# Kernel tuning notes

Hardware: AMD Instinct MI355X
Metric: run time of the kernel (lower is better)

## Reference

```python
import jax, jax.numpy as jnp
import numpy as np
from jax.ops import segment_sum

N_NODES = 100000
N_EDGES = 1600000
IN_DIM, HID_DIM, OUT_DIM = 64, 48, 32


def setup_inputs() -> dict:
    key = jax.random.key(0)
    ks = jax.random.split(key, 4)
    x = jax.random.normal(ks[0], (N_NODES, IN_DIM), dtype=jnp.float32)
    edge_index = jax.random.randint(ks[1], (2, N_EDGES), 0, N_NODES, dtype=jnp.int64)
    W1 = jax.random.normal(ks[2], (IN_DIM, HID_DIM), dtype=jnp.float32) / np.sqrt(IN_DIM)
    b1 = jnp.zeros((HID_DIM,), dtype=jnp.float32)
    W2 = jax.random.normal(ks[3], (HID_DIM, OUT_DIM), dtype=jnp.float32) / np.sqrt(HID_DIM)
    b2 = jnp.zeros((OUT_DIM,), dtype=jnp.float32)
    return {"x": x, "edge_index": edge_index, "W1": W1, "b1": b1, "W2": W2, "b2": b2}


def _gcn_conv(x, W, b, src, dst, deg_inv_sqrt, n_nodes):
    # GCNConv: out = D^{-1/2} (A + I) D^{-1/2} (x W) + b
    h = x @ W                                   # [N, F_out]
    norm = deg_inv_sqrt[src] * deg_inv_sqrt[dst]  # [E+N]
    msg = h[src] * norm[:, None]                # gather + scale
    out = segment_sum(msg, dst, num_segments=n_nodes)  # scatter-add over dst
    return out + b


def reference(x, edge_index, W1, b1, W2, b2):
    n = x.shape[0]
    loop = jnp.arange(n, dtype=edge_index.dtype)
    src = jnp.concatenate([edge_index[0], loop])  # add self-loops (PyG default)
    dst = jnp.concatenate([edge_index[1], loop])
    deg = segment_sum(jnp.ones_like(dst, dtype=x.dtype), dst, num_segments=n)
    deg_inv_sqrt = jnp.where(deg > 0, jax.lax.rsqrt(jnp.maximum(deg, 1.0)), 0.0)
    h = _gcn_conv(x, W1, b1, src, dst, deg_inv_sqrt, n)
    h = jax.nn.relu(h)
    embeddings = _gcn_conv(h, W2, b2, src, dst, deg_inv_sqrt, n)
    return embeddings
```

## Files before the change

kernel.cpp:

```cpp
#include <hip/hip_runtime.h>
#include <hip/hip_fp16.h>


#define NN 100000
#define NE 1600000
#define NPB 128
#define NBUCK ((NN + NPB - 1) / NPB)
#define PBITS 17
#define PMASK ((1 << PBITS) - 1)
#define CHB 3
#define CHS 14
#define NKEY (NPB << CHB)
#define CAP 4096
#define UN 8
#define PART_B 512
#define EPT 8
#define RUNW (PART_B * EPT)
#define PART_G ((NE + RUNW - 1) / RUNW)
#define GROWS 256
#define GEMM_G ((NN + GROWS - 1) / GROWS)
#define GB NBUCK

struct alignas(8)  half4 { __half2 lo, hi; };
struct alignas(16) half8 { __half2 a, b, c, d; };

__global__ __launch_bounds__(512) void
k_lsortgemm(const int* __restrict__ src, const int* __restrict__ dst,
            int* __restrict__ runs, unsigned int* __restrict__ seg,
            const float* __restrict__ X, const float* __restrict__ W1,
            __half* __restrict__ Hh) {
    __shared__ int h[NBUCK];
    __shared__ int tsum[512];
    __shared__ int stage[RUNW];
    __shared__ float w[64 * 48];
    int tid = threadIdx.x;

    if (blockIdx.x < PART_G) {
        for (int i = tid; i < NBUCK; i += PART_B) h[i] = 0;
        __syncthreads();
        int ebase = blockIdx.x * RUNW;
        int pw[EPT], pb[EPT];
#pragma unroll
        for (int k = 0; k < EPT; ++k) {
            int e = ebase + k * PART_B + tid;
            if (e < NE) {
                int d = dst[e];
                pb[k] = d >> 7;
                pw[k] = src[e] | ((d & (NPB - 1)) << PBITS);
                atomicAdd(&h[pb[k]], 1);
            } else pb[k] = -1;
        }
        __syncthreads();
        int c0 = 0, c1 = 0;
        if (tid < NBUCK / 2) { c0 = h[2 * tid]; c1 = h[2 * tid + 1]; }
        int loc = c0 + c1;
        tsum[tid] = (tid < NBUCK / 2) ? loc : 0;
        __syncthreads();
        for (int off = 1; off < 512; off <<= 1) {
            int v = (tid >= off) ? tsum[tid - off] : 0;
            __syncthreads();
            tsum[tid] += v;
            __syncthreads();
        }
        if (tid < NBUCK / 2) {
            int base = tsum[tid] - loc;
            seg[(size_t)blockIdx.x * NBUCK + 2 * tid]     = ((unsigned)base << 9) | (unsigned)c0;
            seg[(size_t)blockIdx.x * NBUCK + 2 * tid + 1] = ((unsigned)(base + c0) << 9) | (unsigned)c1;
            h[2 * tid]     = base;
            h[2 * tid + 1] = base + c0;
        }
        __syncthreads();
#pragma unroll
        for (int k = 0; k < EPT; ++k) {
            if (pb[k] >= 0) {
                int r = atomicAdd(&h[pb[k]], 1);
                stage[r] = pw[k];
            }
        }
        __syncthreads();
#pragma unroll
        for (int k = 0; k < EPT; ++k)
            runs[(size_t)blockIdx.x * RUNW + k * PART_B + tid] = stage[k * PART_B + tid];
        return;
    }

    constexpr int NC = 48, CPT = 12, CG = 4, KF4 = 16;
    int R0 = (blockIdx.x - PART_G) * GROWS;
    for (int i = tid; i < 64 * 48; i += 512) w[i] = W1[i];
    __syncthreads();

    int tc = tid % CG, tr = tid / CG;
    int r0 = R0 + 2 * tr, r1 = r0 + 1;
    int c0 = tc * CPT;
    bool ok0 = r0 < NN, ok1 = r1 < NN;
    const float4* X4 = (const float4*)X;
    const float4 z4 = make_float4(0.f, 0.f, 0.f, 0.f);

    float acc[2][CPT];
#pragma unroll
    for (int rr = 0; rr < 2; ++rr)
#pragma unroll
        for (int j = 0; j < CPT; ++j) acc[rr][j] = 0.f;

#pragma unroll 2
    for (int k4 = 0; k4 < KF4; ++k4) {
        float4 xa = ok0 ? X4[(size_t)r0 * KF4 + k4] : z4;
        float4 xb = ok1 ? X4[(size_t)r1 * KF4 + k4] : z4;
        float ar[4] = {xa.x, xa.y, xa.z, xa.w};
        float br[4] = {xb.x, xb.y, xb.z, xb.w};
#pragma unroll
        for (int j = 0; j < 4; ++j) {
            float va = ar[j], vb = br[j];
#pragma unroll
            for (int q = 0; q < CPT / 4; ++q) {
                float4 wv = *(const float4*)&w[(4 * k4 + j) * NC + c0 + 4 * q];
                acc[0][q*4+0] = fmaf(va, wv.x, acc[0][q*4+0]);
                acc[0][q*4+1] = fmaf(va, wv.y, acc[0][q*4+1]);
                acc[0][q*4+2] = fmaf(va, wv.z, acc[0][q*4+2]);
                acc[0][q*4+3] = fmaf(va, wv.w, acc[0][q*4+3]);
                acc[1][q*4+0] = fmaf(vb, wv.x, acc[1][q*4+0]);
                acc[1][q*4+1] = fmaf(vb, wv.y, acc[1][q*4+1]);
                acc[1][q*4+2] = fmaf(vb, wv.z, acc[1][q*4+2]);
                acc[1][q*4+3] = fmaf(vb, wv.w, acc[1][q*4+3]);
            }
        }
    }
#pragma unroll
    for (int rr = 0; rr < 2; ++rr) {
        int gr = r0 + rr;
        if (gr >= NN) continue;
#pragma unroll
        for (int q = 0; q < CPT / 4; ++q) {
            __half2 p0 = __floats2half2_rn(acc[rr][q*4+0], acc[rr][q*4+1]);
            __half2 p1 = __floats2half2_rn(acc[rr][q*4+2], acc[rr][q*4+3]);
            half4 hv; hv.lo = p0; hv.hi = p1;
            *(half4*)(Hh + (size_t)gr * NC + c0 + 4 * q) = hv;
        }
    }
}

__global__ __launch_bounds__(256) void
k_segt(const unsigned int* __restrict__ seg, unsigned int* __restrict__ segT) {
    __shared__ unsigned int t[32][33];
    constexpr int TX = (NBUCK + 31) / 32;
    int bx = blockIdx.x % TX;
    int by = blockIdx.x / TX;
    int lx = threadIdx.x & 31, ly = threadIdx.x >> 5;
    int bu0 = bx * 32, bl0 = by * 32;
#pragma unroll
    for (int k = 0; k < 32; k += 8) {
        int blk = bl0 + ly + k, bu = bu0 + lx;
        t[ly + k][lx] = (blk < PART_G && bu < NBUCK) ? seg[(size_t)blk * NBUCK + bu] : 0u;
    }
    __syncthreads();
#pragma unroll
    for (int k = 0; k < 32; k += 8) {
        int bu = bu0 + ly + k, blk = bl0 + lx;
        if (bu < NBUCK && blk < PART_G)
            segT[(size_t)bu * PART_G + blk] = t[lx][ly + k];
    }
}

__global__ __launch_bounds__(256) void
k_bsort2(const int* __restrict__ runs, const unsigned int* __restrict__ segT,
         int* __restrict__ srcsort, unsigned int* __restrict__ rowinfo,
         float* __restrict__ dinv, __half* __restrict__ Hh) {
    __shared__ int stage[CAP];
    __shared__ int cnt[NKEY];
    __shared__ int tsum[256];
    __shared__ float sd[NPB];
    int tid = threadIdx.x, b = blockIdx.x;

    unsigned int s0 = (tid < PART_G) ? segT[(size_t)b * PART_G + tid] : 0u;
    unsigned int s1 = (tid + 256 < PART_G) ? segT[(size_t)b * PART_G + tid + 256] : 0u;
    int l0 = (int)(s0 & 511u), l1 = (int)(s1 & 511u);
    int mylen = l0 + l1;
    tsum[tid] = mylen;
    __syncthreads();
    for (int off = 1; off < 256; off <<= 1) {
        int v = (tid >= off) ? tsum[tid - off] : 0;
        __syncthreads();
        tsum[tid] += v;
        __syncthreads();
    }
    int wbase = tsum[tid] - mylen;
    int sz = tsum[255];
    {
        const int* p = runs + (size_t)tid * RUNW + (s0 >> 9);
        for (int i = 0; i < l0; ++i) stage[wbase + i] = p[i];
        p = runs + (size_t)(tid + 256) * RUNW + (s1 >> 9);
        for (int i = 0; i < l1; ++i) stage[wbase + l0 + i] = p[i];
    }
    for (int i = tid; i < NKEY; i += 256) cnt[i] = 0;
    __syncthreads();

    for (int i = tid; i < sz; i += 256) {
        int w = stage[i];
        int key = ((w >> PBITS) << CHB) | ((w & PMASK) >> CHS);
        atomicAdd(&cnt[key], 1);
    }
    __syncthreads();
    int k0 = tid * 4;
    int c0 = cnt[k0], c1 = cnt[k0 + 1], c2 = cnt[k0 + 2], c3 = cnt[k0 + 3];
    int loc = c0 + c1 + c2 + c3;
    tsum[tid] = loc;
    __syncthreads();
    for (int off = 1; off < 256; off <<= 1) {
        int v = (tid >= off) ? tsum[tid - off] : 0;
        __syncthreads();
        tsum[tid] += v;
        __syncthreads();
    }
    int base = tsum[tid] - loc;
    cnt[k0]     = base;
    cnt[k0 + 1] = base + c0;
    cnt[k0 + 2] = base + c0 + c1;
    cnt[k0 + 3] = base + c0 + c1 + c2;
    __syncthreads();
    int e0 = b * CAP;
    if (tid < NPB) {
        int node = b * NPB + tid;
        int rs = cnt[tid << CHB];
        int re = (tid == NPB - 1) ? sz : cnt[(tid + 1) << CHB];
        float dv = rsqrtf((float)(re - rs + 1));
        sd[tid] = dv;
        if (node < NN) {
            rowinfo[node] = ((unsigned int)(e0 + rs) << 10) | (unsigned int)(re - rs);
            dinv[node] = dv;
        }
    }
    __syncthreads();
    for (int i = tid; i < sz; i += 256) {
        int w = stage[i];
        int key = ((w >> PBITS) << CHB) | ((w & PMASK) >> CHS);
        int p = atomicAdd(&cnt[key], 1);
        srcsort[e0 + p] = w & PMASK;
    }
    for (int t = tid; t < NPB * 6; t += 256) {
        int lr = t / 6, q = t - lr * 6;
        int node = b * NPB + lr;
        if (node >= NN) continue;
        float s = sd[lr];
        half8* hp = (half8*)(Hh + (size_t)node * 48 + 8 * q);
        half8 v = *hp;
        float2 f0 = __half22float2(v.a), f1 = __half22float2(v.b);
        float2 f2 = __half22float2(v.c), f3 = __half22float2(v.d);
        v.a = __floats2half2_rn(f0.x * s, f0.y * s);
        v.b = __floats2half2_rn(f1.x * s, f1.y * s);
        v.c = __floats2half2_rn(f2.x * s, f2.y * s);
        v.d = __floats2half2_rn(f3.x * s, f3.y * s);
        *hp = v;
    }
}

__global__ __launch_bounds__(256) void
k_fused48(const __half* __restrict__ Hh, const unsigned int* __restrict__ rowinfo,
          const int* __restrict__ srcsort, const float* __restrict__ dinv,
          const float* __restrict__ b1, const float* __restrict__ W2,
          __half* __restrict__ Hh2) {
    constexpr int ROWS = 128, XS = 49;
    __shared__ float Xs[ROWS * XS];
    __shared__ float w2[48 * 32];
    __shared__ float bb[48];
    int tid = threadIdx.x;
    int R0 = blockIdx.x * ROWS;
    for (int i = tid; i < 48 * 32; i += 256) w2[i] = W2[i];
    if (tid < 48) bb[tid] = b1[tid];
    __syncthreads();

    for (int t = tid; t < ROWS * 6; t += 256) {
        int lr = t / 6, q = t - lr * 6;
        int r = R0 + lr;
        if (r >= NN) continue;
        half8 sv = *(const half8*)(Hh + (size_t)r * 48 + 8 * q);
        float2 f0 = __half22float2(sv.a), f1 = __half22float2(sv.b);
        float2 f2 = __half22float2(sv.c), f3 = __half22float2(sv.d);
        float a0 = f0.x, a1 = f0.y, a2 = f1.x, a3 = f1.y;
        float a4 = f2.x, a5 = f2.y, a6 = f3.x, a7 = f3.y;
        unsigned int rp = rowinfo[r];
        int e0 = rp >> 10, e1 = e0 + (int)(rp & 1023);
        for (int e = e0; e < e1; e += UN) {
            int ss[UN]; float ms[UN];
#pragma unroll
            for (int u = 0; u < UN; ++u) {
                int ee = e + u;
                bool ok = ee < e1;
                ss[u] = srcsort[ok ? ee : e0];
                ms[u] = ok ? 1.f : 0.f;
            }
            half8 vv[UN];
#pragma unroll
            for (int u = 0; u < UN; ++u)
                vv[u] = *(const half8*)(Hh + (size_t)ss[u] * 48 + 8 * q);
#pragma unroll
            for (int u = 0; u < UN; ++u) {
                float2 g0 = __half22float2(vv[u].a), g1 = __half22float2(vv[u].b);
                float2 g2 = __half22float2(vv[u].c), g3 = __half22float2(vv[u].d);
                float m = ms[u];
                a0 = fmaf(g0.x, m, a0); a1 = fmaf(g0.y, m, a1);
                a2 = fmaf(g1.x, m, a2); a3 = fmaf(g1.y, m, a3);
                a4 = fmaf(g2.x, m, a4); a5 = fmaf(g2.y, m, a5);
                a6 = fmaf(g3.x, m, a6); a7 = fmaf(g3.y, m, a7);
            }
        }
        float d = dinv[r];
        float* xr = &Xs[lr * XS + 8 * q];
        const float* bf = &bb[8 * q];
        xr[0] = fmaxf(fmaf(a0, d, bf[0]), 0.f);
        xr[1] = fmaxf(fmaf(a1, d, bf[1]), 0.f);
        xr[2] = fmaxf(fmaf(a2, d, bf[2]), 0.f);
        xr[3] = fmaxf(fmaf(a3, d, bf[3]), 0.f);
        xr[4] = fmaxf(fmaf(a4, d, bf[4]), 0.f);
        xr[5] = fmaxf(fmaf(a5, d, bf[5]), 0.f);
        xr[6] = fmaxf(fmaf(a6, d, bf[6]), 0.f);
        xr[7] = fmaxf(fmaf(a7, d, bf[7]), 0.f);
    }
    __syncthreads();

    int tc = tid & 3, tr = tid >> 2;
    int r0l = 2 * tr, c0 = tc * 8;
    float acc[2][8];
#pragma unroll
    for (int rr = 0; rr < 2; ++rr)
#pragma unroll
        for (int j = 0; j < 8; ++j) acc[rr][j] = 0.f;
#pragma unroll 4
    for (int k = 0; k < 48; ++k) {
        float x0 = Xs[r0l * XS + k];
        float x1 = Xs[(r0l + 1) * XS + k];
        float4 wv0 = *(const float4*)&w2[k * 32 + c0];
        float4 wv1 = *(const float4*)&w2[k * 32 + c0 + 4];
        acc[0][0] = fmaf(x0, wv0.x, acc[0][0]); acc[0][1] = fmaf(x0, wv0.y, acc[0][1]);
        acc[0][2] = fmaf(x0, wv0.z, acc[0][2]); acc[0][3] = fmaf(x0, wv0.w, acc[0][3]);
        acc[0][4] = fmaf(x0, wv1.x, acc[0][4]); acc[0][5] = fmaf(x0, wv1.y, acc[0][5]);
        acc[0][6] = fmaf(x0, wv1.z, acc[0][6]); acc[0][7] = fmaf(x0, wv1.w, acc[0][7]);
        acc[1][0] = fmaf(x1, wv0.x, acc[1][0]); acc[1][1] = fmaf(x1, wv0.y, acc[1][1]);
        acc[1][2] = fmaf(x1, wv0.z, acc[1][2]); acc[1][3] = fmaf(x1, wv0.w, acc[1][3]);
        acc[1][4] = fmaf(x1, wv1.x, acc[1][4]); acc[1][5] = fmaf(x1, wv1.y, acc[1][5]);
        acc[1][6] = fmaf(x1, wv1.z, acc[1][6]); acc[1][7] = fmaf(x1, wv1.w, acc[1][7]);
    }
#pragma unroll
    for (int rr = 0; rr < 2; ++rr) {
        int gr = R0 + r0l + rr;
        if (gr >= NN) continue;
        float d = dinv[gr];
        __half2 p0 = __floats2half2_rn(acc[rr][0] * d, acc[rr][1] * d);
        __half2 p1 = __floats2half2_rn(acc[rr][2] * d, acc[rr][3] * d);
        __half2 p2 = __floats2half2_rn(acc[rr][4] * d, acc[rr][5] * d);
        __half2 p3 = __floats2half2_rn(acc[rr][6] * d, acc[rr][7] * d);
        half8 hv; hv.a = p0; hv.b = p1; hv.c = p2; hv.d = p3;
        *(half8*)(Hh2 + (size_t)gr * 32 + c0) = hv;
    }
}

template <int NC>
__global__ void k_agg(const __half* __restrict__ Hh, const unsigned int* __restrict__ rowinfo,
                      const int* __restrict__ srcsort, const float* __restrict__ dinv,
                      const float* __restrict__ bias, float* __restrict__ out) {
    constexpr int Q = NC / 8;
    int idx = blockIdx.x * blockDim.x + threadIdx.x;
    if (idx >= NN * Q) return;
    int r = idx / Q, q = idx - r * Q;
    half8 sv = *(const half8*)(Hh + (size_t)r * NC + 8 * q);
    float2 f0 = __half22float2(sv.a), f1 = __half22float2(sv.b);
    float2 f2 = __half22float2(sv.c), f3 = __half22float2(sv.d);
    float a0 = f0.x, a1 = f0.y, a2 = f1.x, a3 = f1.y;
    float a4 = f2.x, a5 = f2.y, a6 = f3.x, a7 = f3.y;
    unsigned int rp = rowinfo[r];
    int e0 = rp >> 10, e1 = e0 + (int)(rp & 1023);
    for (int e = e0; e < e1; e += UN) {
        int ss[UN]; float ms[UN];
#pragma unroll
        for (int u = 0; u < UN; ++u) {
            int ee = e + u;
            bool ok = ee < e1;
            ss[u] = srcsort[ok ? ee : e0];
            ms[u] = ok ? 1.f : 0.f;
        }
        half8 vv[UN];
#pragma unroll
        for (int u = 0; u < UN; ++u)
            vv[u] = *(const half8*)(Hh + (size_t)ss[u] * NC + 8 * q);
#pragma unroll
        for (int u = 0; u < UN; ++u) {
            float2 g0 = __half22float2(vv[u].a), g1 = __half22float2(vv[u].b);
            float2 g2 = __half22float2(vv[u].c), g3 = __half22float2(vv[u].d);
            float m = ms[u];
            a0 = fmaf(g0.x, m, a0); a1 = fmaf(g0.y, m, a1);
            a2 = fmaf(g1.x, m, a2); a3 = fmaf(g1.y, m, a3);
            a4 = fmaf(g2.x, m, a4); a5 = fmaf(g2.y, m, a5);
            a6 = fmaf(g3.x, m, a6); a7 = fmaf(g3.y, m, a7);
        }
    }
    float d = dinv[r];
    const float4* b4 = (const float4*)bias;
    float4 bv0 = b4[2 * q], bv1 = b4[2 * q + 1];
    a0 = fmaf(a0, d, bv0.x); a1 = fmaf(a1, d, bv0.y);
    a2 = fmaf(a2, d, bv0.z); a3 = fmaf(a3, d, bv0.w);
    a4 = fmaf(a4, d, bv1.x); a5 = fmaf(a5, d, bv1.y);
    a6 = fmaf(a6, d, bv1.z); a7 = fmaf(a7, d, bv1.w);
    float4* o4 = (float4*)(out + (size_t)r * NC + 8 * q);
    o4[0] = make_float4(a0, a1, a2, a3);
    o4[1] = make_float4(a4, a5, a6, a7);
}

extern "C" void kernel_launch(void* const* d_in, const int* in_sizes, int n_in,
                              void* d_out, int out_size, void* d_ws, size_t ws_size,
                              hipStream_t stream) {
    const float* x  = (const float*)d_in[0];
    const int*   ei = (const int*)d_in[1];
    const float* W1 = (const float*)d_in[2];
    const float* b1 = (const float*)d_in[3];
    const float* W2 = (const float*)d_in[4];
    const float* b2 = (const float*)d_in[5];
    float* out = (float*)d_out;

    const int* src = ei;
    const int* dst = ei + NE;

    char* p = (char*)d_ws;
    auto take = [&](size_t elems) { void* q = p; p += ((elems * 4 + 255) & ~255ull); return q; };
    unsigned int* rowinfo = (unsigned int*)take(NN);
    float*        dinv    = (float*)take(NN);
    int*          srcsort = (int*)take((size_t)NBUCK * CAP);
    __half*       Hh      = (__half*)take((size_t)NN * 24);
    unsigned int* seg     = (unsigned int*)take((size_t)PART_G * NBUCK);
    unsigned int* segT    = (unsigned int*)take((size_t)PART_G * NBUCK);
    int*          runs    = (int*)take((size_t)PART_G * RUNW);
    __half*       Hh2     = (__half*)runs;

    const int B = 256;
    constexpr int SEGT_G = ((NBUCK + 31) / 32) * ((PART_G + 31) / 32);
    k_lsortgemm<<<PART_G + GEMM_G, PART_B, 0, stream>>>(src, dst, runs, seg, x, W1, Hh);
    k_segt<<<SEGT_G, 256, 0, stream>>>(seg, segT);
    k_bsort2<<<NBUCK, 256, 0, stream>>>(runs, segT, srcsort, rowinfo, dinv, Hh);
    k_fused48<<<GB, 256, 0, stream>>>(Hh, rowinfo, srcsort, dinv, b1, W2, Hh2);
    k_agg<32><<<(NN * 4 + B - 1) / B, B, 0, stream>>>(Hh2, rowinfo, srcsort, dinv, b2, out);
}
```

Baseline: 198.8 us.

## Fuse sort, layer fusion and aggregation into persistent kernel with grid barriers

Replaces the transpose, bucket-sort, fused layer-1 aggregation/GEMM and final aggregation kernels with one persistent kernel of NBUCK blocks. The stages are separated by software grid barriers built on an atomic counter, which the previous kernel resets. The segment-table transpose is dropped and per-bucket counts are read with strided accesses instead. This targets launch overheads and inter-kernel gaps. In exchange it relies on all blocks being co-resident and adds barrier spin time and less coalesced seg reads.

New measurement: 653.8 us. 3.29x slower.

```diff
diff --git a/kernel.cpp b/kernel.cpp
--- a/kernel.cpp
+++ b/kernel.cpp
@@ -19,21 +19,46 @@
 #define PART_G ((NE + RUNW - 1) / RUNW)
 #define GROWS 256
 #define GEMM_G ((NN + GROWS - 1) / GROWS)
-#define GB NBUCK
 
 struct alignas(8)  half4 { __half2 lo, hi; };
 struct alignas(16) half8 { __half2 a, b, c, d; };
+
+struct LdsSort {
+    int stage[CAP];
+    int cnt[NKEY];
+    int tsum[256];
+    float sd[NPB];
+};
+struct LdsFused {
+    float Xs[128 * 49];
+    float w2[48 * 32];
+    float bb[48];
+};
+union MegaLds { LdsSort s; LdsFused f; };
+
+__device__ __forceinline__ void gbarrier(int* bar) {
+    __syncthreads();
+    if (threadIdx.x == 0) {
+        __threadfence();
+        __hip_atomic_fetch_add(bar, 1, __ATOMIC_RELEASE, __HIP_MEMORY_SCOPE_AGENT);
+        while (__hip_atomic_load(bar, __ATOMIC_ACQUIRE, __HIP_MEMORY_SCOPE_AGENT) < NBUCK)
+            __builtin_amdgcn_s_sleep(2);
+    }
+    __syncthreads();
+    __threadfence();
+}
 
 __global__ __launch_bounds__(512) void
 k_lsortgemm(const int* __restrict__ src, const int* __restrict__ dst,
             int* __restrict__ runs, unsigned int* __restrict__ seg,
             const float* __restrict__ X, const float* __restrict__ W1,
-            __half* __restrict__ Hh) {
+            __half* __restrict__ Hh, int* __restrict__ gbar) {
     __shared__ int h[NBUCK];
     __shared__ int tsum[512];
     __shared__ int stage[RUNW];
     __shared__ float w[64 * 48];
     int tid = threadIdx.x;
+    if (blockIdx.x == 0 && tid < 2) gbar[tid] = 0;
 
     if (blockIdx.x < PART_G) {
         for (int i = tid; i < NBUCK; i += PART_B) h[i] = 0;
@@ -139,269 +164,240 @@
     }
 }
 
-__global__ __launch_bounds__(256) void
-k_segt(const unsigned int* __restrict__ seg, unsigned int* __restrict__ segT) {
-    __shared__ unsigned int t[32][33];
-    constexpr int TX = (NBUCK + 31) / 32;
-    int bx = blockIdx.x % TX;
-    int by = blockIdx.x / TX;
-    int lx = threadIdx.x & 31, ly = threadIdx.x >> 5;
-    int bu0 = bx * 32, bl0 = by * 32;
-#pragma unroll
-    for (int k = 0; k < 32; k += 8) {
-        int blk = bl0 + ly + k, bu = bu0 + lx;
-        t[ly + k][lx] = (blk < PART_G && bu < NBUCK) ? seg[(size_t)blk * NBUCK + bu] : 0u;
-    }
-    __syncthreads();
-#pragma unroll
-    for (int k = 0; k < 32; k += 8) {
-        int bu = bu0 + ly + k, blk = bl0 + lx;
-        if (bu < NBUCK && blk < PART_G)
-            segT[(size_t)bu * PART_G + blk] = t[lx][ly + k];
-    }
-}
-
-__global__ __launch_bounds__(256) void
-k_bsort2(const int* __restrict__ runs, const unsigned int* __restrict__ segT,
-         int* __restrict__ srcsort, unsigned int* __restrict__ rowinfo,
-         float* __restrict__ dinv, __half* __restrict__ Hh) {
-    __shared__ int stage[CAP];
-    __shared__ int cnt[NKEY];
-    __shared__ int tsum[256];
-    __shared__ float sd[NPB];
+__global__ __launch_bounds__(256, 4) void
+k_mega(const int* __restrict__ runs, const unsigned int* __restrict__ seg,
+       int* __restrict__ srcsort, unsigned int* __restrict__ rowinfo,
+       float* __restrict__ dinv, __half* __restrict__ Hh,
+       const float* __restrict__ b1, const float* __restrict__ W2,
+       __half* __restrict__ Hh2, const float* __restrict__ b2,
+       float* __restrict__ out, int* __restrict__ gbar) {
+    __shared__ MegaLds U;
     int tid = threadIdx.x, b = blockIdx.x;
 
-    unsigned int s0 = (tid < PART_G) ? segT[(size_t)b * PART_G + tid] : 0u;
-    unsigned int s1 = (tid + 256 < PART_G) ? segT[(size_t)b * PART_G + tid + 256] : 0u;
-    int l0 = (int)(s0 & 511u), l1 = (int)(s1 & 511u);
-    int mylen = l0 + l1;
-    tsum[tid] = mylen;
-    __syncthreads();
-    for (int off = 1; off < 256; off <<= 1) {
-        int v = (tid >= off) ? tsum[tid - off] : 0;
-        __syncthreads();
-        tsum[tid] += v;
-        __syncthreads();
-    }
-    int wbase = tsum[tid] - mylen;
-    int sz = tsum[255];
     {
-        const int* p = runs + (size_t)tid * RUNW + (s0 >> 9);
-        for (int i = 0; i < l0; ++i) stage[wbase + i] = p[i];
-        p = runs + (size_t)(tid + 256) * RUNW + (s1 >> 9);
-        for (int i = 0; i < l1; ++i) stage[wbase + l0 + i] = p[i];
-    }
-    for (int i = tid; i < NKEY; i += 256) cnt[i] = 0;
-    __syncthreads();
-
-    for (int i = tid; i < sz; i += 256) {
-        int w = stage[i];
-        int key = ((w >> PBITS) << CHB) | ((w & PMASK) >> CHS);
-        atomicAdd(&cnt[key], 1);
-    }
-    __syncthreads();
-    int k0 = tid * 4;
-    int c0 = cnt[k0], c1 = cnt[k0 + 1], c2 = cnt[k0 + 2], c3 = cnt[k0 + 3];
-    int loc = c0 + c1 + c2 + c3;
-    tsum[tid] = loc;
-    __syncthreads();
-    for (int off = 1; off < 256; off <<= 1) {
-        int v = (tid >= off) ? tsum[tid - off] : 0;
-        __syncthreads();
-        tsum[tid] += v;
-        __syncthreads();
-    }
-    int base = tsum[tid] - loc;
-    cnt[k0]     = base;
-    cnt[k0 + 1] = base + c0;
-    cnt[k0 + 2] = base + c0 + c1;
-    cnt[k0 + 3] = base + c0 + c1 + c2;
-    __syncthreads();
-    int e0 = b * CAP;
-    if (tid < NPB) {
-        int node = b * NPB + tid;
-        int rs = cnt[tid << CHB];
-        int re = (tid == NPB - 1) ? sz : cnt[(tid + 1) << CHB];
-        float dv = rsqrtf((float)(re - rs + 1));
-        sd[tid] = dv;
-        if (node < NN) {
-            rowinfo[node] = ((unsigned int)(e0 + rs) << 10) | (unsigned int)(re - rs);
-            dinv[node] = dv;
-        }
-    }
-    __syncthreads();
-    for (int i = tid; i < sz; i += 256) {
-        int w = stage[i];
-        int key = ((w >> PBITS) << CHB) | ((w & PMASK) >> CHS);
-        int p = atomicAdd(&cnt[key], 1);
-        srcsort[e0 + p] = w & PMASK;
-    }
-    for (int t = tid; t < NPB * 6; t += 256) {
-        int lr = t / 6, q = t - lr * 6;
-        int node = b * NPB + lr;
-        if (node >= NN) continue;
-        float s = sd[lr];
-        half8* hp = (half8*)(Hh + (size_t)node * 48 + 8 * q);
-        half8 v = *hp;
-        float2 f0 = __half22float2(v.a), f1 = __half22float2(v.b);
-        float2 f2 = __half22float2(v.c), f3 = __half22float2(v.d);
-        v.a = __floats2half2_rn(f0.x * s, f0.y * s);
-        v.b = __floats2half2_rn(f1.x * s, f1.y * s);
-        v.c = __floats2half2_rn(f2.x * s, f2.y * s);
-        v.d = __floats2half2_rn(f3.x * s, f3.y * s);
-        *hp = v;
-    }
-}
-
-__global__ __launch_bounds__(256) void
-k_fused48(const __half* __restrict__ Hh, const unsigned int* __restrict__ rowinfo,
-          const int* __restrict__ srcsort, const float* __restrict__ dinv,
-          const float* __restrict__ b1, const float* __restrict__ W2,
-          __half* __restrict__ Hh2) {
-    constexpr int ROWS = 128, XS = 49;
-    __shared__ float Xs[ROWS * XS];
-    __shared__ float w2[48 * 32];
-    __shared__ float bb[48];
-    int tid = threadIdx.x;
-    int R0 = blockIdx.x * ROWS;
-    for (int i = tid; i < 48 * 32; i += 256) w2[i] = W2[i];
-    if (tid < 48) bb[tid] = b1[tid];
-    __syncthreads();
-
-    for (int t = tid; t < ROWS * 6; t += 256) {
-        int lr = t / 6, q = t - lr * 6;
-        int r = R0 + lr;
-        if (r >= NN) continue;
-        half8 sv = *(const half8*)(Hh + (size_t)r * 48 + 8 * q);
-        float2 f0 = __half22float2(sv.a), f1 = __half22float2(sv.b);
-        float2 f2 = __half22float2(sv.c), f3 = __half22float2(sv.d);
-        float a0 = f0.x, a1 = f0.y, a2 = f1.x, a3 = f1.y;
-        float a4 = f2.x, a5 = f2.y, a6 = f3.x, a7 = f3.y;
-        unsigned int rp = rowinfo[r];
-        int e0 = rp >> 10, e1 = e0 + (int)(rp & 1023);
-        for (int e = e0; e < e1; e += UN) {
-            int ss[UN]; float ms[UN];
-#pragma unroll
-            for (int u = 0; u < UN; ++u) {
-                int ee = e + u;
-                bool ok = ee < e1;
-                ss[u] = srcsort[ok ? ee : e0];
-                ms[u] = ok ? 1.f : 0.f;
+        unsigned int s0 = (tid < PART_G) ? seg[(size_t)tid * NBUCK + b] : 0u;
+        unsigned int s1 = (tid + 256 < PART_G) ? seg[(size_t)(tid + 256) * NBUCK + b] : 0u;
+        int l0 = (int)(s0 & 511u), l1 = (int)(s1 & 511u);
+        int mylen = l0 + l1;
+        U.s.tsum[tid] = mylen;
+        __syncthreads();
+        for (int off = 1; off < 256; off <<= 1) {
+            int v = (tid >= off) ? U.s.tsum[tid - off] : 0;
+            __syncthreads();
+            U.s.tsum[tid] += v;
+            __syncthreads();
+        }
+        int wbase = U.s.tsum[tid] - mylen;
+        int sz = U.s.tsum[255];
+        {
+            const int* p = runs + (size_t)tid * RUNW + (s0 >> 9);
+            for (int i = 0; i < l0; ++i) U.s.stage[wbase + i] = p[i];
+            p = runs + (size_t)(tid + 256) * RUNW + (s1 >> 9);
+            for (int i = 0; i < l1; ++i) U.s.stage[wbase + l0 + i] = p[i];
+        }
+        for (int i = tid; i < NKEY; i += 256) U.s.cnt[i] = 0;
+        __syncthreads();
+        for (int i = tid; i < sz; i += 256) {
+            int w = U.s.stage[i];
+            int key = ((w >> PBITS) << CHB) | ((w & PMASK) >> CHS);
+            atomicAdd(&U.s.cnt[key], 1);
+        }
+        __syncthreads();
+        int k0 = tid * 4;
+        int c0 = U.s.cnt[k0], c1 = U.s.cnt[k0 + 1];
+        int c2 = U.s.cnt[k0 + 2], c3 = U.s.cnt[k0 + 3];
+        int loc = c0 + c1 + c2 + c3;
+        U.s.tsum[tid] = loc;
+        __syncthreads();
+        for (int off = 1; off < 256; off <<= 1) {
+            int v = (tid >= off) ? U.s.tsum[tid - off] : 0;
+            __syncthreads();
+            U.s.tsum[tid] += v;
+            __syncthreads();
+        }
+        int base = U.s.tsum[tid] - loc;
+        U.s.cnt[k0]     = base;
+        U.s.cnt[k0 + 1] = base + c0;
+        U.s.cnt[k0 + 2] = base + c0 + c1;
+        U.s.cnt[k0 + 3] = base + c0 + c1 + c2;
+        __syncthreads();
+        int e0 = b * CAP;
+        if (tid < NPB) {
+            int node = b * NPB + tid;
+            int rs = U.s.cnt[tid << CHB];
+            int re = (tid == NPB - 1) ? sz : U.s.cnt[(tid + 1) << CHB];
+            float dv = rsqrtf((float)(re - rs + 1));
+            U.s.sd[tid] = dv;
+            if (node < NN) {
+                rowinfo[node] = ((unsigned int)(e0 + rs) << 10) | (unsigned int)(re - rs);
+                dinv[node] = dv;
             }
-            half8 vv[UN];
-#pragma unroll
-            for (int u = 0; u < UN; ++u)
-                vv[u] = *(const half8*)(Hh + (size_t)ss[u] * 48 + 8 * q);
-#pragma unroll
-            for (int u = 0; u < UN; ++u) {
-                float2 g0 = __half22float2(vv[u].a), g1 = __half22float2(vv[u].b);
-                float2 g2 = __half22float2(vv[u].c), g3 = __half22float2(vv[u].d);
-                float m = ms[u];
-                a0 = fmaf(g0.x, m, a0); a1 = fmaf(g0.y, m, a1);
-                a2 = fmaf(g1.x, m, a2); a3 = fmaf(g1.y, m, a3);
-                a4 = fmaf(g2.x, m, a4); a5 = fmaf(g2.y, m, a5);
-                a6 = fmaf(g3.x, m, a6); a7 = fmaf(g3.y, m, a7);
+        }
+        __syncthreads();
+        for (int i = tid; i < sz; i += 256) {
+            int w = U.s.stage[i];
+            int key = ((w >> PBITS) << CHB) | ((w & PMASK) >> CHS);
+            int p = atomicAdd(&U.s.cnt[key], 1);
+            srcsort[e0 + p] = w & PMASK;
+        }
+        for (int t = tid; t < NPB * 6; t += 256) {
+            int lr = t / 6, q = t - lr * 6;
+            int node = b * NPB + lr;
+            if (node >= NN) continue;
+            float s = U.s.sd[lr];
+            half8* hp = (half8*)(Hh + (size_t)node * 48 + 8 * q);
+            half8 v = *hp;
+            float2 f0 = __half22float2(v.a), f1 = __half22float2(v.b);
+            float2 f2 = __half22float2(v.c), f3 = __half22float2(v.d);
+            v.a = __floats2half2_rn(f0.x * s, f0.y * s);
+            v.b = __floats2half2_rn(f1.x * s, f1.y * s);
+            v.c = __floats2half2_rn(f2.x * s, f2.y * s);
+            v.d = __floats2half2_rn(f3.x * s, f3.y * s);
+            *hp = v;
+        }
+    }
+    gbarrier(&gbar[0]);
+
+    {
+        constexpr int ROWS = 128, XS = 49;
+        int R0 = b * ROWS;
+        for (int i = tid; i < 48 * 32; i += 256) U.f.w2[i] = W2[i];
+        if (tid < 48) U.f.bb[tid] = b1[tid];
+        __syncthreads();
+
+        for (int t = tid; t < ROWS * 6; t += 256) {
+            int lr = t / 6, q = t - lr * 6;
+            int r = R0 + lr;
+            if (r >= NN) continue;
+            half8 sv = *(const half8*)(Hh + (size_t)r * 48 + 8 * q);
+            float2 f0 = __half22float2(sv.a), f1 = __half22float2(sv.b);
+            float2 f2 = __half22float2(sv.c), f3 = __half22float2(sv.d);
+            float a0 = f0.x, a1 = f0.y, a2 = f1.x, a3 = f1.y;
+            float a4 = f2.x, a5 = f2.y, a6 = f3.x, a7 = f3.y;
+            unsigned int rp = rowinfo[r];
+            int e0 = rp >> 10, e1 = e0 + (int)(rp & 1023);
+            for (int e = e0; e < e1; e += UN) {
+                int ss[UN]; float ms[UN];
+#pragma unroll
+                for (int u = 0; u < UN; ++u) {
+                    int ee = e + u;
+                    bool ok = ee < e1;
+                    ss[u] = srcsort[ok ? ee : e0];
+                    ms[u] = ok ? 1.f : 0.f;
+                }
+                half8 vv[UN];
+#pragma unroll
+                for (int u = 0; u < UN; ++u)
+                    vv[u] = *(const half8*)(Hh + (size_t)ss[u] * 48 + 8 * q);
+#pragma unroll
+                for (int u = 0; u < UN; ++u) {
+                    float2 g0 = __half22float2(vv[u].a), g1 = __half22float2(vv[u].b);
+                    float2 g2 = __half22float2(vv[u].c), g3 = __half22float2(vv[u].d);
+                    float m = ms[u];
+                    a0 = fmaf(g0.x, m, a0); a1 = fmaf(g0.y, m, a1);
+                    a2 = fmaf(g1.x, m, a2); a3 = fmaf(g1.y, m, a3);
+                    a4 = fmaf(g2.x, m, a4); a5 = fmaf(g2.y, m, a5);
+                    a6 = fmaf(g3.x, m, a6); a7 = fmaf(g3.y, m, a7);
+                }
             }
-        }
-        float d = dinv[r];
-        float* xr = &Xs[lr * XS + 8 * q];
-        const float* bf = &bb[8 * q];
-        xr[0] = fmaxf(fmaf(a0, d, bf[0]), 0.f);
-        xr[1] = fmaxf(fmaf(a1, d, bf[1]), 0.f);
-        xr[2] = fmaxf(fmaf(a2, d, bf[2]), 0.f);
-        xr[3] = fmaxf(fmaf(a3, d, bf[3]), 0.f);
-        xr[4] = fmaxf(fmaf(a4, d, bf[4]), 0.f);
-        xr[5] = fmaxf(fmaf(a5, d, bf[5]), 0.f);
-        xr[6] = fmaxf(fmaf(a6, d, bf[6]), 0.f);
-        xr[7] = fmaxf(fmaf(a7, d, bf[7]), 0.f);
-    }
-    __syncthreads();
-
-    int tc = tid & 3, tr = tid >> 2;
-    int r0l = 2 * tr, c0 = tc * 8;
-    float acc[2][8];
-#pragma unroll
-    for (int rr = 0; rr < 2; ++rr)
-#pragma unroll
-        for (int j = 0; j < 8; ++j) acc[rr][j] = 0.f;
+            float d = dinv[r];
+            float* xr = &U.f.Xs[lr * XS + 8 * q];
+            const float* bf = &U.f.bb[8 * q];
+            xr[0] = fmaxf(fmaf(a0, d, bf[0]), 0.f);
+            xr[1] = fmaxf(fmaf(a1, d, bf[1]), 0.f);
+            xr[2] = fmaxf(fmaf(a2, d, bf[2]), 0.f);
+            xr[3] = fmaxf(fmaf(a3, d, bf[3]), 0.f);
+            xr[4] = fmaxf(fmaf(a4, d, bf[4]), 0.f);
+            xr[5] = fmaxf(fmaf(a5, d, bf[5]), 0.f);
+            xr[6] = fmaxf(fmaf(a6, d, bf[6]), 0.f);
+            xr[7] = fmaxf(fmaf(a7, d, bf[7]), 0.f);
+        }
+        __syncthreads();
+
+        int tc = tid & 3, tr = tid >> 2;
+        int r0l = 2 * tr, c0 = tc * 8;
+        float acc[2][8];
+#pragma unroll
+        for (int rr = 0; rr < 2; ++rr)
+#pragma unroll
+            for (int j = 0; j < 8; ++j) acc[rr][j] = 0.f;
 #pragma unroll 4
-    for (int k = 0; k < 48; ++k) {
-        float x0 = Xs[r0l * XS + k];
-        float x1 = Xs[(r0l + 1) * XS + k];
-        float4 wv0 = *(const float4*)&w2[k * 32 + c0];
-        float4 wv1 = *(const float4*)&w2[k * 32 + c0 + 4];
-        acc[0][0] = fmaf(x0, wv0.x, acc[0][0]); acc[0][1] = fmaf(x0, wv0.y, acc[0][1]);
-        acc[0][2] = fmaf(x0, wv0.z, acc[0][2]); acc[0][3] = fmaf(x0, wv0.w, acc[0][3]);
-        acc[0][4] = fmaf(x0, wv1.x, acc[0][4]); acc[0][5] = fmaf(x0, wv1.y, acc[0][5]);
-        acc[0][6] = fmaf(x0, wv1.z, acc[0][6]); acc[0][7] = fmaf(x0, wv1.w, acc[0][7]);
-        acc[1][0] = fmaf(x1, wv0.x, acc[1][0]); acc[1][1] = fmaf(x1, wv0.y, acc[1][1]);
-        acc[1][2] = fmaf(x1, wv0.z, acc[1][2]); acc[1][3] = fmaf(x1, wv0.w, acc[1][3]);
-        acc[1][4] = fmaf(x1, wv1.x, acc[1][4]); acc[1][5] = fmaf(x1, wv1.y, acc[1][5]);
-        acc[1][6] = fmaf(x1, wv1.z, acc[1][6]); acc[1][7] = fmaf(x1, wv1.w, acc[1][7]);
-    }
-#pragma unroll
-    for (int rr = 0; rr < 2; ++rr) {
-        int gr = R0 + r0l + rr;
-        if (gr >= NN) continue;
-        float d = dinv[gr];
-        __half2 p0 = __floats2half2_rn(acc[rr][0] * d, acc[rr][1] * d);
-        __half2 p1 = __floats2half2_rn(acc[rr][2] * d, acc[rr][3] * d);
-        __half2 p2 = __floats2half2_rn(acc[rr][4] * d, acc[rr][5] * d);
-        __half2 p3 = __floats2half2_rn(acc[rr][6] * d, acc[rr][7] * d);
-        half8 hv; hv.a = p0; hv.b = p1; hv.c = p2; hv.d = p3;
-        *(half8*)(Hh2 + (size_t)gr * 32 + c0) = hv;
-    }
-}
-
-template <int NC>
-__global__ void k_agg(const __half* __restrict__ Hh, const unsigned int* __restrict__ rowinfo,
-                      const int* __restrict__ srcsort, const float* __restrict__ dinv,
-                      const float* __restrict__ bias, float* __restrict__ out) {
-    constexpr int Q = NC / 8;
-    int idx = blockIdx.x * blockDim.x + threadIdx.x;
-    if (idx >= NN * Q) return;
-    int r = idx / Q, q = idx - r * Q;
-    half8 sv = *(const half8*)(Hh + (size_t)r * NC + 8 * q);
-    float2 f0 = __half22float2(sv.a), f1 = __half22float2(sv.b);
-    float2 f2 = __half22float2(sv.c), f3 = __half22float2(sv.d);
-    float a0 = f0.x, a1 = f0.y, a2 = f1.x, a3 = f1.y;
-    float a4 = f2.x, a5 = f2.y, a6 = f3.x, a7 = f3.y;
-    unsigned int rp = rowinfo[r];
-    int e0 = rp >> 10, e1 = e0 + (int)(rp & 1023);
-    for (int e = e0; e < e1; e += UN) {
-        int ss[UN]; float ms[UN];
-#pragma unroll
-        for (int u = 0; u < UN; ++u) {
-            int ee = e + u;
-            bool ok = ee < e1;
-            ss[u] = srcsort[ok ? ee : e0];
-            ms[u] = ok ? 1.f : 0.f;
-        }
-        half8 vv[UN];
-#pragma unroll
-        for (int u = 0; u < UN; ++u)
-            vv[u] = *(const half8*)(Hh + (size_t)ss[u] * NC + 8 * q);
-#pragma unroll
-        for (int u = 0; u < UN; ++u) {
-            float2 g0 = __half22float2(vv[u].a), g1 = __half22float2(vv[u].b);
-            float2 g2 = __half22float2(vv[u].c), g3 = __half22float2(vv[u].d);
-            float m = ms[u];
-            a0 = fmaf(g0.x, m, a0); a1 = fmaf(g0.y, m, a1);
-            a2 = fmaf(g1.x, m, a2); a3 = fmaf(g1.y, m, a3);
-            a4 = fmaf(g2.x, m, a4); a5 = fmaf(g2.y, m, a5);
-            a6 = fmaf(g3.x, m, a6); a7 = fmaf(g3.y, m, a7);
-        }
-    }
-    float d = dinv[r];
-    const float4* b4 = (const float4*)bias;
-    float4 bv0 = b4[2 * q], bv1 = b4[2 * q + 1];
-    a0 = fmaf(a0, d, bv0.x); a1 = fmaf(a1, d, bv0.y);
-    a2 = fmaf(a2, d, bv0.z); a3 = fmaf(a3, d, bv0.w);
-    a4 = fmaf(a4, d, bv1.x); a5 = fmaf(a5, d, bv1.y);
-    a6 = fmaf(a6, d, bv1.z); a7 = fmaf(a7, d, bv1.w);
-    float4* o4 = (float4*)(out + (size_t)r * NC + 8 * q);
-    o4[0] = make_float4(a0, a1, a2, a3);
-    o4[1] = make_float4(a4, a5, a6, a7);
+        for (int k = 0; k < 48; ++k) {
+            float x0 = U.f.Xs[r0l * XS + k];
+            float x1 = U.f.Xs[(r0l + 1) * XS + k];
+            float4 wv0 = *(const float4*)&U.f.w2[k * 32 + c0];
+            float4 wv1 = *(const float4*)&U.f.w2[k * 32 + c0 + 4];
+            acc[0][0] = fmaf(x0, wv0.x, acc[0][0]); acc[0][1] = fmaf(x0, wv0.y, acc[0][1]);
+            acc[0][2] = fmaf(x0, wv0.z, acc[0][2]); acc[0][3] = fmaf(x0, wv0.w, acc[0][3]);
+            acc[0][4] = fmaf(x0, wv1.x, acc[0][4]); acc[0][5] = fmaf(x0, wv1.y, acc[0][5]);
+            acc[0][6] = fmaf(x0, wv1.z, acc[0][6]); acc[0][7] = fmaf(x0, wv1.w, acc[0][7]);
+            acc[1][0] = fmaf(x1, wv0.x, acc[1][0]); acc[1][1] = fmaf(x1, wv0.y, acc[1][1]);
+            acc[1][2] = fmaf(x1, wv0.z, acc[1][2]); acc[1][3] = fmaf(x1, wv0.w, acc[1][3]);
+            acc[1][4] = fmaf(x1, wv1.x, acc[1][4]); acc[1][5] = fmaf(x1, wv1.y, acc[1][5]);
+            acc[1][6] = fmaf(x1, wv1.z, acc[1][6]); acc[1][7] = fmaf(x1, wv1.w, acc[1][7]);
+        }
+#pragma unroll
+        for (int rr = 0; rr < 2; ++rr) {
+            int gr = R0 + r0l + rr;
+            if (gr >= NN) continue;
+            float d = dinv[gr];
+            __half2 p0 = __floats2half2_rn(acc[rr][0] * d, acc[rr][1] * d);
+            __half2 p1 = __floats2half2_rn(acc[rr][2] * d, acc[rr][3] * d);
+            __half2 p2 = __floats2half2_rn(acc[rr][4] * d, acc[rr][5] * d);
+            __half2 p3 = __floats2half2_rn(acc[rr][6] * d, acc[rr][7] * d);
+            half8 hv; hv.a = p0; hv.b = p1; hv.c = p2; hv.d = p3;
+            *(half8*)(Hh2 + (size_t)gr * 32 + c0) = hv;
+        }
+    }
+    gbarrier(&gbar[1]);
+
+    {
+        constexpr int NC = 32, Q = NC / 8;
+        for (int idx = b * 256 + tid; idx < NN * Q; idx += NBUCK * 256) {
+            int r = idx / Q, q = idx - r * Q;
+            half8 sv = *(const half8*)(Hh2 + (size_t)r * NC + 8 * q);
+            float2 f0 = __half22float2(sv.a), f1 = __half22float2(sv.b);
+            float2 f2 = __half22float2(sv.c), f3 = __half22float2(sv.d);
+            float a0 = f0.x, a1 = f0.y, a2 = f1.x, a3 = f1.y;
+            float a4 = f2.x, a5 = f2.y, a6 = f3.x, a7 = f3.y;
+            unsigned int rp = rowinfo[r];
+            int e0 = rp >> 10, e1 = e0 + (int)(rp & 1023);
+            for (int e = e0; e < e1; e += UN) {
+                int ss[UN]; float ms[UN];
+#pragma unroll
+                for (int u = 0; u < UN; ++u) {
+                    int ee = e + u;
+                    bool ok = ee < e1;
+                    ss[u] = srcsort[ok ? ee : e0];
+                    ms[u] = ok ? 1.f : 0.f;
+                }
+                half8 vv[UN];
+#pragma unroll
+                for (int u = 0; u < UN; ++u)
+                    vv[u] = *(const half8*)(Hh2 + (size_t)ss[u] * NC + 8 * q);
+#pragma unroll
+                for (int u = 0; u < UN; ++u) {
+                    float2 g0 = __half22float2(vv[u].a), g1 = __half22float2(vv[u].b);
+                    float2 g2 = __half22float2(vv[u].c), g3 = __half22float2(vv[u].d);
+                    float m = ms[u];
+                    a0 = fmaf(g0.x, m, a0); a1 = fmaf(g0.y, m, a1);
+                    a2 = fmaf(g1.x, m, a2); a3 = fmaf(g1.y, m, a3);
+                    a4 = fmaf(g2.x, m, a4); a5 = fmaf(g2.y, m, a5);
+                    a6 = fmaf(g3.x, m, a6); a7 = fmaf(g3.y, m, a7);
+                }
+            }
+            float d = dinv[r];
+            const float4* b4 = (const float4*)b2;
+            float4 bv0 = b4[2 * q], bv1 = b4[2 * q + 1];
+            a0 = fmaf(a0, d, bv0.x); a1 = fmaf(a1, d, bv0.y);
+            a2 = fmaf(a2, d, bv0.z); a3 = fmaf(a3, d, bv0.w);
+            a4 = fmaf(a4, d, bv1.x); a5 = fmaf(a5, d, bv1.y);
+            a6 = fmaf(a6, d, bv1.z); a7 = fmaf(a7, d, bv1.w);
+            float4* o4 = (float4*)(out + (size_t)r * NC + 8 * q);
+            o4[0] = make_float4(a0, a1, a2, a3);
+            o4[1] = make_float4(a4, a5, a6, a7);
+        }
+    }
 }
 
 extern "C" void kernel_launch(void* const* d_in, const int* in_sizes, int n_in,
@@ -425,15 +421,11 @@
     int*          srcsort = (int*)take((size_t)NBUCK * CAP);
     __half*       Hh      = (__half*)take((size_t)NN * 24);
     unsigned int* seg     = (unsigned int*)take((size_t)PART_G * NBUCK);
-    unsigned int* segT    = (unsigned int*)take((size_t)PART_G * NBUCK);
+    int*          gbar    = (int*)take(2);
     int*          runs    = (int*)take((size_t)PART_G * RUNW);
     __half*       Hh2     = (__half*)runs;
 
-    const int B = 256;
-    constexpr int SEGT_G = ((NBUCK + 31) / 32) * ((PART_G + 31) / 32);
-    k_lsortgemm<<<PART_G + GEMM_G, PART_B, 0, stream>>>(src, dst, runs, seg, x, W1, Hh);
-    k_segt<<<SEGT_G, 256, 0, stream>>>(seg, segT);
-    k_bsort2<<<NBUCK, 256, 0, stream>>>(runs, segT, srcsort, rowinfo, dinv, Hh);
-    k_fused48<<<GB, 256, 0, stream>>>(Hh, rowinfo, srcsort, dinv, b1, W2, Hh2);
-    k_agg<32><<<(NN * 4 + B - 1) / B, B, 0, stream>>>(Hh2, rowinfo, srcsort, dinv, b2, out);
+    k_lsortgemm<<<PART_G + GEMM_G, PART_B, 0, stream>>>(src, dst, runs, seg, x, W1, Hh, gbar);
+    k_mega<<<NBUCK, 256, 0, stream>>>(runs, seg, srcsort, rowinfo, dinv, Hh,
+                                      b1, W2, Hh2, b2, out, gbar);
 }
```
